# Optimization experiments

Hardware: AMD Instinct MI355X
Metric: run time of the kernel (lower is better)

The kernel has to match this reference:

```python
import jax, jax.numpy as jnp
import numpy as np

EPS = 1e-5


def setup_inputs() -> dict:
    key = jax.random.key(0)
    ks = jax.random.split(key, 5)
    B, C, H, W = 64, 512, 28, 28
    G = 8
    c_half = C // (2 * G)  # 32
    return {
        "x": jax.random.normal(ks[0], (B, C, H, W), dtype=jnp.float32),
        "cweight": jax.random.normal(ks[1], (c_half,), dtype=jnp.float32),
        "cbias": jax.random.normal(ks[2], (c_half,), dtype=jnp.float32),
        "sweight": jax.random.normal(ks[3], (c_half,), dtype=jnp.float32),
        "sbias": jax.random.normal(ks[4], (c_half,), dtype=jnp.float32),
        "G": G,
    }


def reference(x, cweight, cbias, sweight, sbias, G):
    B, C, H, W = x.shape
    HW = H * W
    Cg = C // G
    c_half = Cg // 2

    # group view: [B*G, Cg, HW]
    xg = x.reshape(B * G, Cg, HW)
    x0 = xg[:, :c_half]   # channel-attention half
    x1 = xg[:, c_half:]   # spatial-attention half

    # channel attention: sigmoid(cweight * avgpool_hw(x0) + cbias), per channel
    m = jnp.mean(x0, axis=-1, keepdims=True)                    # [BG, c_half, 1]
    a0 = jax.nn.sigmoid(cweight[None, :, None] * m + cbias[None, :, None])
    y0 = x0 * a0

    # spatial attention: GN stats over the whole c_half*HW slab per (b,g)
    mu = jnp.mean(x1, axis=(1, 2), keepdims=True)               # [BG, 1, 1]
    var = jnp.mean(x1 * x1, axis=(1, 2), keepdims=True) - mu * mu
    rstd = jax.lax.rsqrt(jnp.maximum(var, 0.0) + EPS)
    norm = (x1 - mu) * rstd
    a1 = jax.nn.sigmoid(sweight[None, :, None] * norm + sbias[None, :, None])
    y1 = x1 * a1

    y = jnp.concatenate([y0, y1], axis=1).reshape(B, C, HW)

    # channel shuffle with 2 groups: out[:, 2*w + g2] = y[:, g2*(C//2) + w]
    y = y.reshape(B, 2, C // 2, HW).transpose(0, 2, 1, 3).reshape(B, C, H, W)
    return y
```

## Files before the change

### kernel.cpp

```cpp
#include <hip/hip_runtime.h>

#define EPSV 1e-5f

__device__ __forceinline__ float sigmoidf_(float z) {
    return 1.0f / (1.0f + __expf(-z));
}

__global__ __launch_bounds__(512, 4) void stats_kernel(
    const float4* __restrict__ x4,
    const float* __restrict__ cweight,
    const float* __restrict__ cbias,
    float* __restrict__ ws)
{
    const int bg  = blockIdx.x;
    const int tid = threadIdx.x;
    const int cc  = tid >> 3;
    const int ts  = tid & 7;

    const float4* __restrict__ xch = x4 + (size_t)bg * (64 * 196) + cc * 196;

    float s = 0.f, ss = 0.f;
#pragma unroll
    for (int k = 0; k < 24; ++k) {
        float4 v = xch[ts + 8 * k];
        s  += (v.x + v.y) + (v.z + v.w);
        ss += (v.x * v.x + v.y * v.y) + (v.z * v.z + v.w * v.w);
    }
    if (ts < 4) {
        float4 v = xch[192 + ts];
        s  += (v.x + v.y) + (v.z + v.w);
        ss += (v.x * v.x + v.y * v.y) + (v.z * v.z + v.w * v.w);
    }

    s  += __shfl_xor(s, 1, 64);  s  += __shfl_xor(s, 2, 64);  s  += __shfl_xor(s, 4, 64);
    ss += __shfl_xor(ss, 1, 64); ss += __shfl_xor(ss, 2, 64); ss += __shfl_xor(ss, 4, 64);

    __shared__ float lds_s[4];
    __shared__ float lds_ss[4];

    if (cc < 32) {
        if (ts == 0) {
            const float mean = s * (1.0f / 784.0f);
            ws[(size_t)bg * 34 + cc] = sigmoidf_(cweight[cc] * mean + cbias[cc]);
        }
    } else {
        s  += __shfl_xor(s, 8, 64);  s  += __shfl_xor(s, 16, 64);  s  += __shfl_xor(s, 32, 64);
        ss += __shfl_xor(ss, 8, 64); ss += __shfl_xor(ss, 16, 64); ss += __shfl_xor(ss, 32, 64);
        const int w = (tid >> 6) - 4;
        if ((tid & 63) == 0) { lds_s[w] = s; lds_ss[w] = ss; }
    }
    __syncthreads();
    if (tid == 0) {
        const float S  = (lds_s[0] + lds_s[1]) + (lds_s[2] + lds_s[3]);
        const float SS = (lds_ss[0] + lds_ss[1]) + (lds_ss[2] + lds_ss[3]);
        constexpr float inv_n = 1.0f / (32.0f * 784.0f);
        const float mu   = S * inv_n;
        const float var  = SS * inv_n - mu * mu;
        const float rstd = rsqrtf(fmaxf(var, 0.f) + EPSV);
        ws[(size_t)bg * 34 + 32] = mu;
        ws[(size_t)bg * 34 + 33] = rstd;
    }
}

__global__ __launch_bounds__(256, 8) void apply_kernel(
    const float4* __restrict__ x4,
    const float* __restrict__ sweight,
    const float* __restrict__ sbias,
    const float* __restrict__ ws,
    float4* __restrict__ out4,
    int total4)
{
    for (int i = blockIdx.x * 256 + threadIdx.x; i < total4;
         i += gridDim.x * 256) {
        const int bg  = i / 12544;
        const int rem = i - bg * 12544;
        const int cc  = rem / 196;
        const int p   = rem - cc * 196;

        const float4 v = x4[i];
        float4 r;
        if (cc < 32) {
            const float a0 = ws[(size_t)bg * 34 + cc];
            r.x = v.x * a0; r.y = v.y * a0; r.z = v.z * a0; r.w = v.w * a0;
        } else {
            const float mu   = ws[(size_t)bg * 34 + 32];
            const float rstd = ws[(size_t)bg * 34 + 33];
            const float w    = sweight[cc - 32];
            const float bch  = sbias[cc - 32];
            r.x = v.x * sigmoidf_(w * ((v.x - mu) * rstd) + bch);
            r.y = v.y * sigmoidf_(w * ((v.y - mu) * rstd) + bch);
            r.z = v.z * sigmoidf_(w * ((v.z - mu) * rstd) + bch);
            r.w = v.w * sigmoidf_(w * ((v.w - mu) * rstd) + bch);
        }

        const int b  = bg >> 3;
        const int g  = bg & 7;
        const int c  = g * 64 + cc;
        const int cp = (c < 256) ? (2 * c) : (2 * (c - 256) + 1);
        out4[(size_t)b * 100352 + (size_t)cp * 196 + p] = r;
    }
}

extern "C" void kernel_launch(void* const* d_in, const int* in_sizes, int n_in,
                              void* d_out, int out_size, void* d_ws, size_t ws_size,
                              hipStream_t stream) {
    const float* x  = (const float*)d_in[0];
    const float* cw = (const float*)d_in[1];
    const float* cb = (const float*)d_in[2];
    const float* sw = (const float*)d_in[3];
    const float* sb = (const float*)d_in[4];
    float* out = (float*)d_out;
    float* ws  = (float*)d_ws;

    const int B = in_sizes[0] / (512 * 784);
    const int nbg = B * 8;
    const int total4 = B * 512 * 196;

    stats_kernel<<<nbg, 512, 0, stream>>>(
        (const float4*)x, cw, cb, ws);

    const int apply_blocks = 2048;
    apply_kernel<<<apply_blocks, 256, 0, stream>>>(
        (const float4*)x, sw, sb, ws, (float4*)out, total4);
}
```

Measured before the change: 204.9 us.

## Fuse channel-attention half into stats pass and fold GN affine into per-channel coefficients

The channel-attention half is now computed and written in the first kernel: one wavefront per channel holds its data in registers, reduces it, and scales it directly. The x0 half is no longer re-read in a second pass. The stats blocks for the spatial half fold mean, rstd, weight and bias into a per-channel A,B pair, so the apply kernel only touches the x1 half with a single FMA before each sigmoid. Stores are nontemporal. The cost is mixing two block roles in one launch and keeping registers per wave for the held data.

```diff
diff --git a/kernel.cpp b/kernel.cpp
--- a/kernel.cpp
+++ b/kernel.cpp
@@ -1,4 +1,7 @@
 #include <hip/hip_runtime.h>
+
+typedef float f32x4 __attribute__((ext_vector_type(4)));
+typedef float f32x2 __attribute__((ext_vector_type(2)));
 
 #define EPSV 1e-5f
 
@@ -6,98 +9,122 @@
     return 1.0f / (1.0f + __expf(-z));
 }
 
-__global__ __launch_bounds__(512, 4) void stats_kernel(
-    const float4* __restrict__ x4,
+__global__ __launch_bounds__(256) void gate_stats_kernel(
+    const f32x4* __restrict__ x4,
     const float* __restrict__ cweight,
     const float* __restrict__ cbias,
-    float* __restrict__ ws)
+    const float* __restrict__ sweight,
+    const float* __restrict__ sbias,
+    f32x4* __restrict__ out4,
+    f32x2* __restrict__ wsAB,
+    int nA)
 {
-    const int bg  = blockIdx.x;
-    const int tid = threadIdx.x;
-    const int cc  = tid >> 3;
-    const int ts  = tid & 7;
+    if ((int)blockIdx.x < nA) {
+        const int w  = blockIdx.x * 4 + (threadIdx.x >> 6);
+        const int ln = threadIdx.x & 63;
+        const int bg = w >> 5;
+        const int cc = w & 31;
 
-    const float4* __restrict__ xch = x4 + (size_t)bg * (64 * 196) + cc * 196;
+        const f32x4* __restrict__ xch = x4 + (size_t)bg * 12544 + cc * 196;
+        f32x4 v0 = xch[ln];
+        f32x4 v1 = xch[64 + ln];
+        f32x4 v2 = xch[128 + ln];
+        f32x4 v3 = {0.f, 0.f, 0.f, 0.f};
+        const bool extra = (ln < 4);
+        if (extra) v3 = xch[192 + ln];
 
-    float s = 0.f, ss = 0.f;
+        float s = (v0.x + v0.y) + (v0.z + v0.w)
+                + (v1.x + v1.y) + (v1.z + v1.w)
+                + (v2.x + v2.y) + (v2.z + v2.w)
+                + (v3.x + v3.y) + (v3.z + v3.w);
 #pragma unroll
-    for (int k = 0; k < 24; ++k) {
-        float4 v = xch[ts + 8 * k];
-        s  += (v.x + v.y) + (v.z + v.w);
-        ss += (v.x * v.x + v.y * v.y) + (v.z * v.z + v.w * v.w);
-    }
-    if (ts < 4) {
-        float4 v = xch[192 + ts];
-        s  += (v.x + v.y) + (v.z + v.w);
-        ss += (v.x * v.x + v.y * v.y) + (v.z * v.z + v.w * v.w);
-    }
+        for (int m = 32; m >= 1; m >>= 1) s += __shfl_xor(s, m, 64);
 
-    s  += __shfl_xor(s, 1, 64);  s  += __shfl_xor(s, 2, 64);  s  += __shfl_xor(s, 4, 64);
-    ss += __shfl_xor(ss, 1, 64); ss += __shfl_xor(ss, 2, 64); ss += __shfl_xor(ss, 4, 64);
+        const float a0 = sigmoidf_(cweight[cc] * (s * (1.0f / 784.0f)) + cbias[cc]);
 
-    __shared__ float lds_s[4];
-    __shared__ float lds_ss[4];
+        const int b = bg >> 3, g = bg & 7;
+        const int c  = g * 64 + cc;
+        const int cp = (c < 256) ? (2 * c) : (2 * (c - 256) + 1);
+        f32x4* __restrict__ och = out4 + (size_t)b * 100352 + (size_t)cp * 196;
 
-    if (cc < 32) {
-        if (ts == 0) {
-            const float mean = s * (1.0f / 784.0f);
-            ws[(size_t)bg * 34 + cc] = sigmoidf_(cweight[cc] * mean + cbias[cc]);
+        __builtin_nontemporal_store(v0 * a0, &och[ln]);
+        __builtin_nontemporal_store(v1 * a0, &och[64 + ln]);
+        __builtin_nontemporal_store(v2 * a0, &och[128 + ln]);
+        if (extra) __builtin_nontemporal_store(v3 * a0, &och[192 + ln]);
+    } else {
+        const int bg  = (int)blockIdx.x - nA;
+        const int tid = threadIdx.x;
+        const f32x4* __restrict__ xs = x4 + (size_t)bg * 12544 + 6272;
+
+        float s = 0.f, ss = 0.f;
+#pragma unroll
+        for (int k = 0; k < 24; ++k) {
+            f32x4 v = xs[tid + 256 * k];
+            s  += (v.x + v.y) + (v.z + v.w);
+            ss += (v.x * v.x + v.y * v.y) + (v.z * v.z + v.w * v.w);
         }
-    } else {
-        s  += __shfl_xor(s, 8, 64);  s  += __shfl_xor(s, 16, 64);  s  += __shfl_xor(s, 32, 64);
-        ss += __shfl_xor(ss, 8, 64); ss += __shfl_xor(ss, 16, 64); ss += __shfl_xor(ss, 32, 64);
-        const int w = (tid >> 6) - 4;
-        if ((tid & 63) == 0) { lds_s[w] = s; lds_ss[w] = ss; }
-    }
-    __syncthreads();
-    if (tid == 0) {
-        const float S  = (lds_s[0] + lds_s[1]) + (lds_s[2] + lds_s[3]);
-        const float SS = (lds_ss[0] + lds_ss[1]) + (lds_ss[2] + lds_ss[3]);
-        constexpr float inv_n = 1.0f / (32.0f * 784.0f);
-        const float mu   = S * inv_n;
-        const float var  = SS * inv_n - mu * mu;
-        const float rstd = rsqrtf(fmaxf(var, 0.f) + EPSV);
-        ws[(size_t)bg * 34 + 32] = mu;
-        ws[(size_t)bg * 34 + 33] = rstd;
+        if (tid < 128) {
+            f32x4 v = xs[6144 + tid];
+            s  += (v.x + v.y) + (v.z + v.w);
+            ss += (v.x * v.x + v.y * v.y) + (v.z * v.z + v.w * v.w);
+        }
+
+#pragma unroll
+        for (int m = 32; m >= 1; m >>= 1) {
+            s  += __shfl_xor(s,  m, 64);
+            ss += __shfl_xor(ss, m, 64);
+        }
+
+        __shared__ float lds_s[4], lds_ss[4], lds_st[2];
+        const int wv = tid >> 6;
+        if ((tid & 63) == 0) { lds_s[wv] = s; lds_ss[wv] = ss; }
+        __syncthreads();
+        if (tid == 0) {
+            const float S  = (lds_s[0] + lds_s[1]) + (lds_s[2] + lds_s[3]);
+            const float SS = (lds_ss[0] + lds_ss[1]) + (lds_ss[2] + lds_ss[3]);
+            constexpr float inv_n = 1.0f / (32.0f * 784.0f);
+            const float mu   = S * inv_n;
+            const float var  = SS * inv_n - mu * mu;
+            const float rstd = rsqrtf(fmaxf(var, 0.f) + EPSV);
+            lds_st[0] = mu; lds_st[1] = rstd;
+        }
+        __syncthreads();
+        if (tid < 32) {
+            const float mu = lds_st[0], rstd = lds_st[1];
+            const float A  = sweight[tid] * rstd;
+            f32x2 ab; ab.x = A; ab.y = sbias[tid] - A * mu;
+            wsAB[bg * 32 + tid] = ab;
+        }
     }
 }
 
-__global__ __launch_bounds__(256, 8) void apply_kernel(
-    const float4* __restrict__ x4,
-    const float* __restrict__ sweight,
-    const float* __restrict__ sbias,
-    const float* __restrict__ ws,
-    float4* __restrict__ out4,
-    int total4)
+__global__ __launch_bounds__(256) void apply1_kernel(
+    const f32x4* __restrict__ x4,
+    const f32x2* __restrict__ wsAB,
+    f32x4* __restrict__ out4,
+    int total)
 {
-    for (int i = blockIdx.x * 256 + threadIdx.x; i < total4;
+    for (int i = blockIdx.x * 256 + threadIdx.x; i < total;
          i += gridDim.x * 256) {
-        const int bg  = i / 12544;
-        const int rem = i - bg * 12544;
-        const int cc  = rem / 196;
-        const int p   = rem - cc * 196;
+        const int bg  = i / 6272;
+        const int rem = i - bg * 6272;
+        const int c1  = rem / 196;
+        const int p   = rem - c1 * 196;
 
-        const float4 v = x4[i];
-        float4 r;
-        if (cc < 32) {
-            const float a0 = ws[(size_t)bg * 34 + cc];
-            r.x = v.x * a0; r.y = v.y * a0; r.z = v.z * a0; r.w = v.w * a0;
-        } else {
-            const float mu   = ws[(size_t)bg * 34 + 32];
-            const float rstd = ws[(size_t)bg * 34 + 33];
-            const float w    = sweight[cc - 32];
-            const float bch  = sbias[cc - 32];
-            r.x = v.x * sigmoidf_(w * ((v.x - mu) * rstd) + bch);
-            r.y = v.y * sigmoidf_(w * ((v.y - mu) * rstd) + bch);
-            r.z = v.z * sigmoidf_(w * ((v.z - mu) * rstd) + bch);
-            r.w = v.w * sigmoidf_(w * ((v.w - mu) * rstd) + bch);
-        }
+        const f32x4 v = x4[(size_t)bg * 12544 + 6272 + rem];
+        const f32x2 ab = wsAB[bg * 32 + c1];
 
-        const int b  = bg >> 3;
-        const int g  = bg & 7;
-        const int c  = g * 64 + cc;
+        f32x4 r;
+        r.x = v.x * sigmoidf_(ab.x * v.x + ab.y);
+        r.y = v.y * sigmoidf_(ab.x * v.y + ab.y);
+        r.z = v.z * sigmoidf_(ab.x * v.z + ab.y);
+        r.w = v.w * sigmoidf_(ab.x * v.w + ab.y);
+
+        const int b = bg >> 3, g = bg & 7;
+        const int c  = g * 64 + 32 + c1;
         const int cp = (c < 256) ? (2 * c) : (2 * (c - 256) + 1);
-        out4[(size_t)b * 100352 + (size_t)cp * 196 + p] = r;
+        __builtin_nontemporal_store(
+            r, out4 + (size_t)b * 100352 + (size_t)cp * 196 + p);
     }
 }
 
@@ -110,16 +137,16 @@
     const float* sw = (const float*)d_in[3];
     const float* sb = (const float*)d_in[4];
     float* out = (float*)d_out;
-    float* ws  = (float*)d_ws;
 
-    const int B = in_sizes[0] / (512 * 784);
-    const int nbg = B * 8;
-    const int total4 = B * 512 * 196;
+    const int B  = in_sizes[0] / (512 * 784);
+    const int nA = B * 64;
+    const int nB = B * 8;
 
-    stats_kernel<<<nbg, 512, 0, stream>>>(
-        (const float4*)x, cw, cb, ws);
+    gate_stats_kernel<<<nA + nB, 256, 0, stream>>>(
+        (const f32x4*)x, cw, cb, sw, sb,
+        (f32x4*)out, (f32x2*)d_ws, nA);
 
-    const int apply_blocks = 2048;
-    apply_kernel<<<apply_blocks, 256, 0, stream>>>(
-        (const float4*)x, sw, sb, ws, (float4*)out, total4);
+    const int total1 = B * 8 * 6272;
+    apply1_kernel<<<2048, 256, 0, stream>>>(
+        (const f32x4*)x, (const f32x2*)d_ws, (f32x4*)out, total1);
 }
```

After: 199.9 us. -2.4%, faster.
